# Optimization experiments

Measured on AMD Instinct MI355X. Metric: run time of the kernel, lower is better.

## Reference

```python
import jax, jax.numpy as jnp
import numpy as np

H, W, C = 1080, 1920, 3


def setup_inputs() -> dict:
    key = jax.random.key(0)
    k1, k2, k3 = jax.random.split(key, 3)
    img = jax.random.normal(k1, (H, W, C), dtype=jnp.float32)
    # ~10px typical displacement for realistic optical flow
    flow = jax.random.normal(k2, (1, H, W, 2), dtype=jnp.float32) * 10.0
    # depths in [0.1, 80); no pixel hits the 100.0 invalid sentinel
    depth = jax.random.uniform(k3, (H, W), dtype=jnp.float32, minval=0.1, maxval=80.0)
    return {"img": img, "flow": flow, "depth": depth, "split": 10}


def reference(img, flow, depth, split):
    # Depth-ordered forward-warping splat (z-buffer style compositing).
    # kernel_size=1 -> nearest-neighbor splat: each source pixel (y,x) writes
    # its value to (round(y+flow_y), round(x+flow_x)); passes go far->near and
    # nearer (nonzero) writes overwrite farther ones.
    flow = flow[0]                      # [H, W, 2], (dx, dy)
    h, w, c = img.shape

    # midpoints of the depth histogram, excluding the 100.0 invalid sentinel
    valid = depth != 100.0
    sd = jnp.sort(jnp.where(valid, depth, jnp.inf).ravel())
    l = valid.sum()
    step = l // split
    mids = jnp.concatenate(
        [jnp.take(sd, jnp.arange(split) * step), jnp.take(sd, l - 1)[None]]
    )  # [split+1], ascending

    ys, xs = jnp.meshgrid(jnp.arange(h), jnp.arange(w), indexing="ij")
    ty = jnp.round(ys + flow[..., 1]).astype(jnp.int32)   # target row
    tx = jnp.round(xs + flow[..., 0]).astype(jnp.int32)   # target col

    res = jnp.zeros_like(img)
    for i in range(split, 0, -1):       # far bin first, near bin last
        dmask = (depth < mids[i]) & (depth >= mids[i - 1])   # [H, W]
        # pixels outside the bin scatter to row h -> dropped (mode='drop')
        ty_i = jnp.where(dmask, ty, h)
        out = jnp.zeros_like(img).at[ty_i, tx].set(
            img * dmask[..., None].astype(img.dtype), mode="drop"
        )
        # nearer nonzero splats overwrite; zeros keep previous content
        res = res * (out == 0) + out
    return res
```

## Files before the change

kernel.cpp:

```cpp
#include <hip/hip_runtime.h>

typedef unsigned int u32;

static constexpr int HH = 1080, WW = 1920;
static constexpr int NPIX = HH * WW;
static constexpr int NQ = 17;
static constexpr int MAXOWN = 16;
static constexpr int OPB = 4;
static constexpr int NGRP = MAXOWN / OPB;
static constexpr int NBLK = 512;
static constexpr int BT   = 1024;
static constexpr int R1 = 16;
static constexpr int NCH1 = 64;
static constexpr int TS = 64;
static constexpr int TCX = WW / TS;
static constexpr int TCY = (HH + TS - 1) / TS;
static constexpr int NTILE = TCX * TCY;
static constexpr int NT512 = 512;

static constexpr size_t MIDS_OFF  = 0;
static constexpr size_t QB1_OFF   = 128;
static constexpr size_t QR1_OFF   = 256;
static constexpr size_t OIDX_OFF  = 384;
static constexpr size_t OBIN_OFF  = 512;
static constexpr size_t NOWN_OFF  = 640;
static constexpr size_t KEY22_OFF = 768;
static constexpr size_t R2O_OFF   = 896;
static constexpr size_t TOT1_OFF  = 1024;
static constexpr size_t GH2_OFF   = TOT1_OFF + (size_t)R1 * 4096 * 4;
static constexpr size_t ZERO_BYTES = GH2_OFF + (size_t)NQ * 1024 * 4;
static constexpr size_t TCNT_OFF  = ZERO_BYTES;
static constexpr size_t TTOT_OFF  = TCNT_OFF + (size_t)NBLK * NT512 * 4;
static constexpr size_t TBASE_OFF = TTOT_OFF + NT512 * 4;
static constexpr size_t TEND_OFF  = TBASE_OFF + NT512 * 4;
static constexpr size_t BASE2_OFF = TEND_OFF + NT512 * 4;
static constexpr size_t GH1_OFF   = BASE2_OFF + (size_t)NBLK * NT512 * 4;
static constexpr size_t PAIRS_OFF = GH1_OFF + (size_t)MAXOWN * NCH1 * 1024 * 4;

static constexpr int ZVEC = (int)(ZERO_BYTES / 16);
static constexpr int ZBLK = (ZVEC + 255) / 256;

__global__ __launch_bounds__(256) void k_zero(float4* __restrict__ ws) {
    int i = blockIdx.x * 256 + threadIdx.x;
    if (i < ZVEC) ws[i] = make_float4(0.f, 0.f, 0.f, 0.f);
}

__device__ __forceinline__ int target_of(int y, int x, float fx, float fy) {
    int ty = (int)rintf((float)y + fy);
    int tx = (int)rintf((float)x + fx);
    if (ty < 0) ty += HH;
    if (tx < 0) tx += WW;
    if ((unsigned)ty >= (unsigned)HH || (unsigned)tx >= (unsigned)WW) return -1;
    return ty * WW + tx;
}

__global__ __launch_bounds__(BT) void k_histA_cnt(const float* __restrict__ depth,
                                                  const float* __restrict__ flow,
                                                  u32* __restrict__ tot1,
                                                  u32* __restrict__ tcnt) {
    __shared__ u32 h[4096];
    __shared__ u32 tc[NT512];
    int tid = threadIdx.x;
    for (int j = tid; j < 4096; j += BT) h[j] = 0;
    for (int j = tid; j < NT512; j += BT) tc[j] = 0;
    __syncthreads();
    const int nvec = NPIX / 4;
    for (int v = blockIdx.x * BT + tid; v < nvec; v += gridDim.x * BT) {
        int i = v * 4;
        float4 d4 = ((const float4*)depth)[v];
        float4 fa = ((const float4*)flow)[v * 2];
        float4 fb = ((const float4*)flow)[v * 2 + 1];
        int y = i / WW, x0 = i - y * WW;
        float dd[4] = {d4.x, d4.y, d4.z, d4.w};
        float fx[4] = {fa.x, fa.z, fb.x, fb.z};
        float fy[4] = {fa.y, fa.w, fb.y, fb.w};
        #pragma unroll
        for (int j = 0; j < 4; ++j) {
            if (dd[j] != 100.0f)
                atomicAdd(&h[__float_as_uint(dd[j]) >> 20], 1u);
            int t = target_of(y, x0 + j, fx[j], fy[j]);
            if (t >= 0) {
                int ty = t / WW, tx = t - ty * WW;
                atomicAdd(&tc[(ty >> 6) * TCX + (tx >> 6)], 1u);
            }
        }
    }
    __syncthreads();
    u32 rep = blockIdx.x & (R1 - 1);
    for (int j = tid; j < 4096; j += BT) {
        u32 v = h[j];
        if (v) atomicAdd(&tot1[rep * 4096 + j], v);
    }
    for (int j = tid; j < NT512; j += BT)
        tcnt[blockIdx.x * NT512 + j] = tc[j];
}

__global__ __launch_bounds__(NBLK) void k_tscan(const u32* __restrict__ tcnt,
                                                u32* __restrict__ ttot,
                                                u32* __restrict__ base2) {
    __shared__ u32 s[NBLK];
    int t = blockIdx.x, b = threadIdx.x;
    u32 v = tcnt[b * NT512 + t];
    s[b] = v;
    __syncthreads();
    for (int off = 1; off < NBLK; off <<= 1) {
        u32 x = (b >= off) ? s[b - off] : 0;
        __syncthreads();
        s[b] += x;
        __syncthreads();
    }
    base2[b * NT512 + t] = s[b] - v;
    if (b == NBLK - 1) ttot[t] = s[NBLK - 1];
}

__global__ __launch_bounds__(1024) void k_selA(const u32* __restrict__ tot1,
                                               const int* __restrict__ splitp,
                                               const u32* __restrict__ ttot,
                                               u32* __restrict__ qb1, u32* __restrict__ qr1,
                                               u32* __restrict__ oidx, u32* __restrict__ obin,
                                               u32* __restrict__ nown,
                                               u32* __restrict__ tbase, u32* __restrict__ tend) {
    __shared__ u32 part[1024];
    __shared__ u32 qbS[NQ], qcS[NQ];
    __shared__ u32 totalsh;
    int tid = threadIdx.x;
    int split = *splitp;
    int base = tid * 4;
    u32 cc[4] = {0, 0, 0, 0};
    for (int r = 0; r < R1; ++r)
        for (int j = 0; j < 4; ++j) cc[j] += tot1[r * 4096 + base + j];
    u32 local = cc[0] + cc[1] + cc[2] + cc[3];
    part[tid] = local;
    __syncthreads();
    for (int off = 1; off < 1024; off <<= 1) {
        u32 v = (tid >= off) ? part[tid - off] : 0;
        __syncthreads();
        part[tid] += v;
        __syncthreads();
    }
    if (tid == 1023) totalsh = part[1023];
    __syncthreads();
    u32 l = totalsh;
    u32 step = l / (u32)split;
    u32 cum = part[tid] - local;
    for (int j = 0; j < 4; ++j) {
        u32 c = cc[j];
        if (c) {
            for (int q = 0; q <= split; ++q) {
                u32 r = (q < split) ? (u32)q * step : l - 1u;
                if (r >= cum && r < cum + c) {
                    qb1[q] = (u32)(base + j);
                    qr1[q] = r - cum;
                    qbS[q] = (u32)(base + j);
                    qcS[q] = c;
                }
            }
        }
        cum += c;
    }
    __syncthreads();
    if (tid == 0) {
        int w = -1;
        u32 prev = 0xFFFFFFFFu;
        for (int q = 0; q <= split; ++q) {
            if (qbS[q] != prev) { ++w; prev = qbS[q]; obin[w] = qbS[q]; }
            oidx[q] = (u32)w;
        }
        for (int w2 = w + 1; w2 < MAXOWN; ++w2) obin[w2] = 0xFFFFFFFFu;
        *nown = (u32)(w + 1);
    }
    __syncthreads();
    u32 tv = (tid < NT512) ? ttot[tid] : 0;
    part[tid] = tv;
    __syncthreads();
    for (int off = 1; off < 1024; off <<= 1) {
        u32 v = (tid >= off) ? part[tid - off] : 0;
        __syncthreads();
        part[tid] += v;
        __syncthreads();
    }
    if (tid < NT512) {
        tbase[tid] = part[tid] - tv;
        tend[tid]  = part[tid];
    }
}

__global__ __launch_bounds__(1024) void k_ph1(const float* __restrict__ depth,
                                              const u32* __restrict__ obin,
                                              const u32* __restrict__ nownp,
                                              u32* __restrict__ ghist) {
    int c = blockIdx.x / NGRP;
    int g = blockIdx.x % NGRP;
    int w0 = g * OPB;
    int nown = (int)*nownp;
    if (w0 >= nown) return;
    __shared__ u32 h[OPB * 1024];
    int tid = threadIdx.x;
    u32 ob[OPB];
    #pragma unroll
    for (int k = 0; k < OPB; ++k)
        ob[k] = (w0 + k < nown) ? obin[w0 + k] : 0xFFFFFFFFu;
    for (int j = tid; j < OPB * 1024; j += 1024) h[j] = 0;
    __syncthreads();
    const int per = (NPIX / 4) / NCH1;
    int lo = c * per, hi = lo + per;
    for (int v = lo + tid; v < hi; v += 1024) {
        float4 d4 = ((const float4*)depth)[v];
        float dd[4] = {d4.x, d4.y, d4.z, d4.w};
        #pragma unroll
        for (int j = 0; j < 4; ++j) {
            u32 bits = __float_as_uint(dd[j]);
            u32 b1 = bits >> 20;
            #pragma unroll
            for (int k = 0; k < OPB; ++k)
                if (ob[k] == b1)
                    atomicAdd(&h[k * 1024 + ((bits >> 10) & 1023u)], 1u);
        }
    }
    __syncthreads();
    for (int j = tid; j < OPB * 1024; j += 1024) {
        int k = j >> 10, bin = j & 1023;
        int w = w0 + k;
        if (w < nown) ghist[(w * NCH1 + c) * 1024 + bin] = h[j];
    }
}

__global__ __launch_bounds__(1024) void k_red1(const int* __restrict__ splitp,
                                               const u32* __restrict__ qb1,
                                               const u32* __restrict__ qr1,
                                               const u32* __restrict__ oidx,
                                               const u32* __restrict__ ghist,
                                               u32* __restrict__ key22, u32* __restrict__ r2o) {
    int q = blockIdx.x;
    if (q > *splitp) return;
    int w = (int)oidx[q];
    __shared__ u32 part[1024];
    int tid = threadIdx.x;
    u32 local = 0;
    for (int c = 0; c < NCH1; ++c) local += ghist[(w * NCH1 + c) * 1024 + tid];
    part[tid] = local;
    __syncthreads();
    for (int off = 1; off < 1024; off <<= 1) {
        u32 v = (tid >= off) ? part[tid - off] : 0;
        __syncthreads();
        part[tid] += v;
        __syncthreads();
    }
    u32 target = qr1[q];
    u32 cum = part[tid] - local;
    if (local && target >= cum && target < cum + local) {
        key22[q] = (qb1[q] << 10) | (u32)tid;
        r2o[q] = target - cum;
    }
}

__global__ __launch_bounds__(256) void k_ph2(const float* __restrict__ depth,
                                             const int* __restrict__ splitp,
                                             const u32* __restrict__ key22,
                                             u32* __restrict__ gh2) {
    __shared__ u32 k22[NQ];
    int tid = threadIdx.x, split = *splitp;
    if (tid < NQ) k22[tid] = (tid <= split) ? key22[tid] : 0xFFFFFFFFu;
    __syncthreads();
    const int nvec = NPIX / 4;
    for (int v = blockIdx.x * blockDim.x + tid; v < nvec; v += gridDim.x * blockDim.x) {
        float4 d4 = ((const float4*)depth)[v];
        float dd[4] = {d4.x, d4.y, d4.z, d4.w};
        #pragma unroll
        for (int j = 0; j < 4; ++j) {
            if (dd[j] != 100.0f) {
                u32 bits = __float_as_uint(dd[j]);
                u32 hi22 = bits >> 10;
                for (int q = 0; q <= split; ++q)
                    if (k22[q] == hi22) atomicAdd(&gh2[q * 1024 + (bits & 1023u)], 1u);
            }
        }
    }
}

__global__ __launch_bounds__(1024) void k_red2(const int* __restrict__ splitp,
                                               const u32* __restrict__ key22,
                                               const u32* __restrict__ r2o,
                                               const u32* __restrict__ gh2,
                                               float* __restrict__ mids) {
    int q = blockIdx.x;
    if (q > *splitp) return;
    __shared__ u32 part[1024];
    int tid = threadIdx.x;
    u32 local = gh2[q * 1024 + tid];
    part[tid] = local;
    __syncthreads();
    for (int off = 1; off < 1024; off <<= 1) {
        u32 v = (tid >= off) ? part[tid - off] : 0;
        __syncthreads();
        part[tid] += v;
        __syncthreads();
    }
    u32 target = r2o[q];
    u32 cum = part[tid] - local;
    if (local && target >= cum && target < cum + local)
        mids[q] = __uint_as_float((key22[q] << 10) | (u32)tid);
}

__global__ __launch_bounds__(BT) void k_scatter(const float* __restrict__ depth,
                                                const float* __restrict__ flow,
                                                const int* __restrict__ splitp,
                                                const float* __restrict__ mids,
                                                const u32* __restrict__ tbase,
                                                const u32* __restrict__ base2,
                                                uint2* __restrict__ pairs) {
    __shared__ u32 cur[NT512];
    __shared__ float msh[NQ];
    int tid = threadIdx.x, split = *splitp;
    if (tid < NQ) msh[tid] = (tid <= split) ? mids[tid] : 0.f;
    for (int j = tid; j < NT512; j += BT)
        cur[j] = tbase[j] + base2[blockIdx.x * NT512 + j];
    __syncthreads();
    const int nvec = NPIX / 4;
    for (int v = blockIdx.x * BT + tid; v < nvec; v += gridDim.x * BT) {
        int i = v * 4;
        float4 d4 = ((const float4*)depth)[v];
        float4 fa = ((const float4*)flow)[v * 2];
        float4 fb = ((const float4*)flow)[v * 2 + 1];
        int y = i / WW, x0 = i - y * WW;
        float dd[4] = {d4.x, d4.y, d4.z, d4.w};
        float fx[4] = {fa.x, fa.z, fb.x, fb.z};
        float fy[4] = {fa.y, fa.w, fb.y, fb.w};
        #pragma unroll
        for (int j = 0; j < 4; ++j) {
            int t = target_of(y, x0 + j, fx[j], fy[j]);
            if (t < 0) continue;
            float d = dd[j];
            int rank = -1;
            for (int k = 1; k <= split; ++k)
                if (d >= msh[k - 1] && d < msh[k]) { rank = split - k; break; }
            u32 p = (rank >= 0) ? (u32)rank * (u32)NPIX + (u32)(i + j) + 1u : 0u;
            int ty = t / WW, tx = t - ty * WW;
            int tile = (ty >> 6) * TCX + (tx >> 6);
            u32 pos = atomicAdd(&cur[tile], 1u);
            pairs[pos] = make_uint2((u32)t, p);
        }
    }
}

__global__ __launch_bounds__(1024) void k_tile_reduce(const uint2* __restrict__ pairs,
                                                      const u32* __restrict__ tbase,
                                                      const u32* __restrict__ tend,
                                                      const float* __restrict__ img,
                                                      float* __restrict__ out) {
    __shared__ u32 zb[TS * TS];
    int tid = threadIdx.x;
    int tile = blockIdx.x;
    for (int c = tid; c < TS * TS; c += 1024) zb[c] = 0;
    __syncthreads();
    int ty0 = (tile / TCX) << 6, tx0 = (tile % TCX) << 6;
    u32 b = tbase[tile], e = tend[tile];
    for (u32 k = b + tid; k < e; k += 1024) {
        uint2 pr = pairs[k];
        int t = (int)pr.x;
        int ty = t / WW, tx = t - ty * WW;
        atomicMax(&zb[((ty - ty0) << 6) | (tx - tx0)], pr.y);
    }
    __syncthreads();
    for (int c = tid; c < TS * TS; c += 1024) {
        int ty = ty0 + (c >> 6);
        if (ty >= HH) continue;
        int tx = tx0 + (c & 63);
        u32 p = zb[c];
        float r = 0.f, g = 0.f, bl = 0.f;
        if (p) {
            u32 src = (p - 1u) % (u32)NPIX;
            r  = img[src * 3 + 0];
            g  = img[src * 3 + 1];
            bl = img[src * 3 + 2];
        }
        int t = ty * WW + tx;
        out[t * 3 + 0] = r;
        out[t * 3 + 1] = g;
        out[t * 3 + 2] = bl;
    }
}

extern "C" void kernel_launch(void* const* d_in, const int* in_sizes, int n_in,
                              void* d_out, int out_size, void* d_ws, size_t ws_size,
                              hipStream_t stream) {
    const float* img    = (const float*)d_in[0];
    const float* flow   = (const float*)d_in[1];
    const float* depth  = (const float*)d_in[2];
    const int*   splitp = (const int*)d_in[3];

    char* ws = (char*)d_ws;
    float* mids  = (float*)(ws + MIDS_OFF);
    u32*   qb1   = (u32*)(ws + QB1_OFF);
    u32*   qr1   = (u32*)(ws + QR1_OFF);
    u32*   oidx  = (u32*)(ws + OIDX_OFF);
    u32*   obin  = (u32*)(ws + OBIN_OFF);
    u32*   nown  = (u32*)(ws + NOWN_OFF);
    u32*   key22 = (u32*)(ws + KEY22_OFF);
    u32*   r2o   = (u32*)(ws + R2O_OFF);
    u32*   tot1  = (u32*)(ws + TOT1_OFF);
    u32*   gh2   = (u32*)(ws + GH2_OFF);
    u32*   tcnt  = (u32*)(ws + TCNT_OFF);
    u32*   ttot  = (u32*)(ws + TTOT_OFF);
    u32*   tbase = (u32*)(ws + TBASE_OFF);
    u32*   tend  = (u32*)(ws + TEND_OFF);
    u32*   base2 = (u32*)(ws + BASE2_OFF);
    u32*   gh1   = (u32*)(ws + GH1_OFF);
    uint2* pairs = (uint2*)(ws + PAIRS_OFF);
    float* out   = (float*)d_out;

    k_zero       <<<ZBLK, 256, 0, stream>>>((float4*)d_ws);
    k_histA_cnt  <<<NBLK, BT, 0, stream>>>(depth, flow, tot1, tcnt);
    k_tscan      <<<NT512, NBLK, 0, stream>>>(tcnt, ttot, base2);
    k_selA       <<<1, 1024, 0, stream>>>(tot1, splitp, ttot, qb1, qr1, oidx, obin, nown, tbase, tend);
    k_ph1        <<<NCH1 * NGRP, 1024, 0, stream>>>(depth, obin, nown, gh1);
    k_red1       <<<NQ, 1024, 0, stream>>>(splitp, qb1, qr1, oidx, gh1, key22, r2o);
    k_ph2        <<<2048, 256, 0, stream>>>(depth, splitp, key22, gh2);
    k_red2       <<<NQ, 1024, 0, stream>>>(splitp, key22, r2o, gh2, mids);
    k_scatter    <<<NBLK, BT, 0, stream>>>(depth, flow, splitp, mids, tbase, base2, pairs);
    k_tile_reduce<<<NTILE, 1024, 0, stream>>>(pairs, tbase, tend, img, out);
}
```

Measured before the change: 95.81 us.

## Fuse tile counting, scan and scatter into per-block staged segments

Drops the separate tile-count pass and global tile scan. Each block now counts its pixels per tile, scans those counts in shared memory, stages its (target, priority) pairs in LDS and writes them to its own fixed segment. The tile reducer then gathers from every block's segment using per-block counts and offsets. This removes one full pass over depth and flow, the scan kernel and the scattered global writes. The price is a serial per-thread loop over segments in the reducer, with only a few threads active per tile, and the ph1 chunking knobs are retuned.

New measurement: 104.2 us. 8.7% more time.

```diff
diff --git a/kernel.cpp b/kernel.cpp
--- a/kernel.cpp
+++ b/kernel.cpp
@@ -4,14 +4,16 @@
 
 static constexpr int HH = 1080, WW = 1920;
 static constexpr int NPIX = HH * WW;
+static constexpr int NVEC = NPIX / 4;
 static constexpr int NQ = 17;
 static constexpr int MAXOWN = 16;
-static constexpr int OPB = 4;
+static constexpr int OPB = 8;
 static constexpr int NGRP = MAXOWN / OPB;
 static constexpr int NBLK = 512;
 static constexpr int BT   = 1024;
+static constexpr int SEG  = 4096;
 static constexpr int R1 = 16;
-static constexpr int NCH1 = 64;
+static constexpr int NCH1 = 128;
 static constexpr int TS = 64;
 static constexpr int TCX = WW / TS;
 static constexpr int TCY = (HH + TS - 1) / TS;
@@ -30,10 +32,7 @@
 static constexpr size_t GH2_OFF   = TOT1_OFF + (size_t)R1 * 4096 * 4;
 static constexpr size_t ZERO_BYTES = GH2_OFF + (size_t)NQ * 1024 * 4;
 static constexpr size_t TCNT_OFF  = ZERO_BYTES;
-static constexpr size_t TTOT_OFF  = TCNT_OFF + (size_t)NBLK * NT512 * 4;
-static constexpr size_t TBASE_OFF = TTOT_OFF + NT512 * 4;
-static constexpr size_t TEND_OFF  = TBASE_OFF + NT512 * 4;
-static constexpr size_t BASE2_OFF = TEND_OFF + NT512 * 4;
+static constexpr size_t BASE2_OFF = TCNT_OFF + (size_t)NBLK * NT512 * 4;
 static constexpr size_t GH1_OFF   = BASE2_OFF + (size_t)NBLK * NT512 * 4;
 static constexpr size_t PAIRS_OFF = GH1_OFF + (size_t)MAXOWN * NCH1 * 1024 * 4;
 
@@ -54,36 +53,19 @@
     return ty * WW + tx;
 }
 
-__global__ __launch_bounds__(BT) void k_histA_cnt(const float* __restrict__ depth,
-                                                  const float* __restrict__ flow,
-                                                  u32* __restrict__ tot1,
-                                                  u32* __restrict__ tcnt) {
+__global__ __launch_bounds__(BT) void k_histQ(const float* __restrict__ depth,
+                                              u32* __restrict__ tot1) {
     __shared__ u32 h[4096];
-    __shared__ u32 tc[NT512];
     int tid = threadIdx.x;
     for (int j = tid; j < 4096; j += BT) h[j] = 0;
-    for (int j = tid; j < NT512; j += BT) tc[j] = 0;
-    __syncthreads();
-    const int nvec = NPIX / 4;
-    for (int v = blockIdx.x * BT + tid; v < nvec; v += gridDim.x * BT) {
-        int i = v * 4;
+    __syncthreads();
+    for (int v = blockIdx.x * BT + tid; v < NVEC; v += gridDim.x * BT) {
         float4 d4 = ((const float4*)depth)[v];
-        float4 fa = ((const float4*)flow)[v * 2];
-        float4 fb = ((const float4*)flow)[v * 2 + 1];
-        int y = i / WW, x0 = i - y * WW;
         float dd[4] = {d4.x, d4.y, d4.z, d4.w};
-        float fx[4] = {fa.x, fa.z, fb.x, fb.z};
-        float fy[4] = {fa.y, fa.w, fb.y, fb.w};
         #pragma unroll
-        for (int j = 0; j < 4; ++j) {
+        for (int j = 0; j < 4; ++j)
             if (dd[j] != 100.0f)
                 atomicAdd(&h[__float_as_uint(dd[j]) >> 20], 1u);
-            int t = target_of(y, x0 + j, fx[j], fy[j]);
-            if (t >= 0) {
-                int ty = t / WW, tx = t - ty * WW;
-                atomicAdd(&tc[(ty >> 6) * TCX + (tx >> 6)], 1u);
-            }
-        }
     }
     __syncthreads();
     u32 rep = blockIdx.x & (R1 - 1);
@@ -91,37 +73,15 @@
         u32 v = h[j];
         if (v) atomicAdd(&tot1[rep * 4096 + j], v);
     }
-    for (int j = tid; j < NT512; j += BT)
-        tcnt[blockIdx.x * NT512 + j] = tc[j];
-}
-
-__global__ __launch_bounds__(NBLK) void k_tscan(const u32* __restrict__ tcnt,
-                                                u32* __restrict__ ttot,
-                                                u32* __restrict__ base2) {
-    __shared__ u32 s[NBLK];
-    int t = blockIdx.x, b = threadIdx.x;
-    u32 v = tcnt[b * NT512 + t];
-    s[b] = v;
-    __syncthreads();
-    for (int off = 1; off < NBLK; off <<= 1) {
-        u32 x = (b >= off) ? s[b - off] : 0;
-        __syncthreads();
-        s[b] += x;
-        __syncthreads();
-    }
-    base2[b * NT512 + t] = s[b] - v;
-    if (b == NBLK - 1) ttot[t] = s[NBLK - 1];
 }
 
 __global__ __launch_bounds__(1024) void k_selA(const u32* __restrict__ tot1,
                                                const int* __restrict__ splitp,
-                                               const u32* __restrict__ ttot,
                                                u32* __restrict__ qb1, u32* __restrict__ qr1,
                                                u32* __restrict__ oidx, u32* __restrict__ obin,
-                                               u32* __restrict__ nown,
-                                               u32* __restrict__ tbase, u32* __restrict__ tend) {
+                                               u32* __restrict__ nown) {
     __shared__ u32 part[1024];
-    __shared__ u32 qbS[NQ], qcS[NQ];
+    __shared__ u32 qbS[NQ];
     __shared__ u32 totalsh;
     int tid = threadIdx.x;
     int split = *splitp;
@@ -152,7 +112,6 @@
                     qb1[q] = (u32)(base + j);
                     qr1[q] = r - cum;
                     qbS[q] = (u32)(base + j);
-                    qcS[q] = c;
                 }
             }
         }
@@ -168,20 +127,6 @@
         }
         for (int w2 = w + 1; w2 < MAXOWN; ++w2) obin[w2] = 0xFFFFFFFFu;
         *nown = (u32)(w + 1);
-    }
-    __syncthreads();
-    u32 tv = (tid < NT512) ? ttot[tid] : 0;
-    part[tid] = tv;
-    __syncthreads();
-    for (int off = 1; off < 1024; off <<= 1) {
-        u32 v = (tid >= off) ? part[tid - off] : 0;
-        __syncthreads();
-        part[tid] += v;
-        __syncthreads();
-    }
-    if (tid < NT512) {
-        tbase[tid] = part[tid] - tv;
-        tend[tid]  = part[tid];
     }
 }
 
@@ -202,7 +147,7 @@
         ob[k] = (w0 + k < nown) ? obin[w0 + k] : 0xFFFFFFFFu;
     for (int j = tid; j < OPB * 1024; j += 1024) h[j] = 0;
     __syncthreads();
-    const int per = (NPIX / 4) / NCH1;
+    const int per = NVEC / NCH1;
     int lo = c * per, hi = lo + per;
     for (int v = lo + tid; v < hi; v += 1024) {
         float4 d4 = ((const float4*)depth)[v];
@@ -262,8 +207,7 @@
     int tid = threadIdx.x, split = *splitp;
     if (tid < NQ) k22[tid] = (tid <= split) ? key22[tid] : 0xFFFFFFFFu;
     __syncthreads();
-    const int nvec = NPIX / 4;
-    for (int v = blockIdx.x * blockDim.x + tid; v < nvec; v += gridDim.x * blockDim.x) {
+    for (int v = blockIdx.x * blockDim.x + tid; v < NVEC; v += gridDim.x * blockDim.x) {
         float4 d4 = ((const float4*)depth)[v];
         float dd[4] = {d4.x, d4.y, d4.z, d4.w};
         #pragma unroll
@@ -302,22 +246,30 @@
         mids[q] = __uint_as_float((key22[q] << 10) | (u32)tid);
 }
 
-__global__ __launch_bounds__(BT) void k_scatter(const float* __restrict__ depth,
-                                                const float* __restrict__ flow,
-                                                const int* __restrict__ splitp,
-                                                const float* __restrict__ mids,
-                                                const u32* __restrict__ tbase,
-                                                const u32* __restrict__ base2,
-                                                uint2* __restrict__ pairs) {
+__global__ __launch_bounds__(BT) void k_build(const float* __restrict__ depth,
+                                              const float* __restrict__ flow,
+                                              const int* __restrict__ splitp,
+                                              const float* __restrict__ mids,
+                                              u32* __restrict__ tcnt,
+                                              u32* __restrict__ base2,
+                                              uint2* __restrict__ pairs) {
+    __shared__ u32 tc[NT512];
+    __shared__ u32 s[NT512];
     __shared__ u32 cur[NT512];
+    __shared__ uint2 stage[SEG];
     __shared__ float msh[NQ];
-    int tid = threadIdx.x, split = *splitp;
+    __shared__ u32 total_sh;
+    int tid = threadIdx.x;
+    int split = *splitp;
     if (tid < NQ) msh[tid] = (tid <= split) ? mids[tid] : 0.f;
-    for (int j = tid; j < NT512; j += BT)
-        cur[j] = tbase[j] + base2[blockIdx.x * NT512 + j];
-    __syncthreads();
-    const int nvec = NPIX / 4;
-    for (int v = blockIdx.x * BT + tid; v < nvec; v += gridDim.x * BT) {
+    if (tid < NT512) tc[tid] = 0;
+    __syncthreads();
+    int v = blockIdx.x * BT + tid;
+    int tt[4];
+    u32 pp[4] = {0, 0, 0, 0};
+    #pragma unroll
+    for (int j = 0; j < 4; ++j) tt[j] = -1;
+    if (v < NVEC) {
         int i = v * 4;
         float4 d4 = ((const float4*)depth)[v];
         float4 fa = ((const float4*)flow)[v * 2];
@@ -329,37 +281,76 @@
         #pragma unroll
         for (int j = 0; j < 4; ++j) {
             int t = target_of(y, x0 + j, fx[j], fy[j]);
-            if (t < 0) continue;
-            float d = dd[j];
-            int rank = -1;
-            for (int k = 1; k <= split; ++k)
-                if (d >= msh[k - 1] && d < msh[k]) { rank = split - k; break; }
-            u32 p = (rank >= 0) ? (u32)rank * (u32)NPIX + (u32)(i + j) + 1u : 0u;
+            tt[j] = t;
+            if (t >= 0) {
+                float d = dd[j];
+                int rank = -1;
+                for (int k = 1; k <= split; ++k)
+                    if (d >= msh[k - 1] && d < msh[k]) { rank = split - k; break; }
+                pp[j] = (rank >= 0) ? (u32)rank * (u32)NPIX + (u32)(i + j) + 1u : 0u;
+                int ty = t / WW, tx = t - ty * WW;
+                atomicAdd(&tc[(ty >> 6) * TCX + (tx >> 6)], 1u);
+            }
+        }
+    }
+    __syncthreads();
+    if (tid < NT512) s[tid] = tc[tid];
+    __syncthreads();
+    for (int off = 1; off < NT512; off <<= 1) {
+        u32 x = (tid < NT512 && tid >= off) ? s[tid - off] : 0;
+        __syncthreads();
+        if (tid < NT512) s[tid] += x;
+        __syncthreads();
+    }
+    if (tid < NT512) {
+        u32 c = tc[tid];
+        u32 b = s[tid] - c;
+        tcnt[blockIdx.x * NT512 + tid]  = c;
+        base2[blockIdx.x * NT512 + tid] = b;
+        cur[tid] = b;
+    }
+    if (tid == NT512 - 1) total_sh = s[NT512 - 1];
+    __syncthreads();
+    #pragma unroll
+    for (int j = 0; j < 4; ++j) {
+        if (tt[j] >= 0) {
+            int t = tt[j];
             int ty = t / WW, tx = t - ty * WW;
-            int tile = (ty >> 6) * TCX + (tx >> 6);
-            u32 pos = atomicAdd(&cur[tile], 1u);
-            pairs[pos] = make_uint2((u32)t, p);
-        }
-    }
+            u32 pos = atomicAdd(&cur[(ty >> 6) * TCX + (tx >> 6)], 1u);
+            stage[pos] = make_uint2((u32)t, pp[j]);
+        }
+    }
+    __syncthreads();
+    u32 total = total_sh;
+    uint2* segp = pairs + (size_t)blockIdx.x * SEG;
+    for (u32 j = tid; j < total; j += BT) segp[j] = stage[j];
 }
 
 __global__ __launch_bounds__(1024) void k_tile_reduce(const uint2* __restrict__ pairs,
-                                                      const u32* __restrict__ tbase,
-                                                      const u32* __restrict__ tend,
+                                                      const u32* __restrict__ tcnt,
+                                                      const u32* __restrict__ base2,
                                                       const float* __restrict__ img,
                                                       float* __restrict__ out) {
     __shared__ u32 zb[TS * TS];
+    __shared__ u32 cnt_l[NT512], off_l[NT512];
     int tid = threadIdx.x;
     int tile = blockIdx.x;
     for (int c = tid; c < TS * TS; c += 1024) zb[c] = 0;
+    if (tid < NT512) {
+        cnt_l[tid] = tcnt[tid * NT512 + tile];
+        off_l[tid] = base2[tid * NT512 + tile];
+    }
     __syncthreads();
     int ty0 = (tile / TCX) << 6, tx0 = (tile % TCX) << 6;
-    u32 b = tbase[tile], e = tend[tile];
-    for (u32 k = b + tid; k < e; k += 1024) {
-        uint2 pr = pairs[k];
-        int t = (int)pr.x;
-        int ty = t / WW, tx = t - ty * WW;
-        atomicMax(&zb[((ty - ty0) << 6) | (tx - tx0)], pr.y);
+    if (tid < NT512) {
+        u32 c = cnt_l[tid];
+        const uint2* segp = pairs + (size_t)tid * SEG + off_l[tid];
+        for (u32 k = 0; k < c; ++k) {
+            uint2 pr = segp[k];
+            int t = (int)pr.x;
+            int ty = t / WW, tx = t - ty * WW;
+            atomicMax(&zb[((ty - ty0) << 6) | (tx - tx0)], pr.y);
+        }
     }
     __syncthreads();
     for (int c = tid; c < TS * TS; c += 1024) {
@@ -401,22 +392,18 @@
     u32*   tot1  = (u32*)(ws + TOT1_OFF);
     u32*   gh2   = (u32*)(ws + GH2_OFF);
     u32*   tcnt  = (u32*)(ws + TCNT_OFF);
-    u32*   ttot  = (u32*)(ws + TTOT_OFF);
-    u32*   tbase = (u32*)(ws + TBASE_OFF);
-    u32*   tend  = (u32*)(ws + TEND_OFF);
     u32*   base2 = (u32*)(ws + BASE2_OFF);
     u32*   gh1   = (u32*)(ws + GH1_OFF);
     uint2* pairs = (uint2*)(ws + PAIRS_OFF);
     float* out   = (float*)d_out;
 
     k_zero       <<<ZBLK, 256, 0, stream>>>((float4*)d_ws);
-    k_histA_cnt  <<<NBLK, BT, 0, stream>>>(depth, flow, tot1, tcnt);
-    k_tscan      <<<NT512, NBLK, 0, stream>>>(tcnt, ttot, base2);
-    k_selA       <<<1, 1024, 0, stream>>>(tot1, splitp, ttot, qb1, qr1, oidx, obin, nown, tbase, tend);
+    k_histQ      <<<NBLK, BT, 0, stream>>>(depth, tot1);
+    k_selA       <<<1, 1024, 0, stream>>>(tot1, splitp, qb1, qr1, oidx, obin, nown);
     k_ph1        <<<NCH1 * NGRP, 1024, 0, stream>>>(depth, obin, nown, gh1);
     k_red1       <<<NQ, 1024, 0, stream>>>(splitp, qb1, qr1, oidx, gh1, key22, r2o);
     k_ph2        <<<2048, 256, 0, stream>>>(depth, splitp, key22, gh2);
     k_red2       <<<NQ, 1024, 0, stream>>>(splitp, key22, r2o, gh2, mids);
-    k_scatter    <<<NBLK, BT, 0, stream>>>(depth, flow, splitp, mids, tbase, base2, pairs);
-    k_tile_reduce<<<NTILE, 1024, 0, stream>>>(pairs, tbase, tend, img, out);
-}
+    k_build      <<<NBLK, BT, 0, stream>>>(depth, flow, splitp, mids, tcnt, base2, pairs);
+    k_tile_reduce<<<NTILE, 1024, 0, stream>>>(pairs, tcnt, base2, img, out);
+}
```

## Merge tile scan with bin selection and move tile-base scan into red1

Applied to the files above, without the earlier changes.

Merges the per-tile prefix-scan kernel and the single-block selection kernel into one launch, where the extra block does the bin selection with 512 threads handling 8 bins each. The global tile-base scan moves into an extra block of the k_red1 launch, so one kernel launch and one serial dependency step are removed. It also retunes phase-1 histogram parameters (8 owners per block, 128 chunks). The gh1 buffer layout changes with NCH1 and must still fit the workspace, and k_red1 now sums twice as many chunks per bin.

Measured after the change: 95.17 us, median of 2. Within noise of the previous version (-0.7%).

```diff
diff --git a/kernel.cpp b/kernel.cpp
--- a/kernel.cpp
+++ b/kernel.cpp
@@ -4,14 +4,16 @@
 
 static constexpr int HH = 1080, WW = 1920;
 static constexpr int NPIX = HH * WW;
+static constexpr int NVEC = NPIX / 4;
 static constexpr int NQ = 17;
 static constexpr int MAXOWN = 16;
-static constexpr int OPB = 4;
+static constexpr int OPB = 8;
 static constexpr int NGRP = MAXOWN / OPB;
 static constexpr int NBLK = 512;
 static constexpr int BT   = 1024;
 static constexpr int R1 = 16;
-static constexpr int NCH1 = 64;
+static constexpr int NCH1 = 128;
+static constexpr int CH1V = NVEC / NCH1;
 static constexpr int TS = 64;
 static constexpr int TCX = WW / TS;
 static constexpr int TCY = (HH + TS - 1) / TS;
@@ -64,8 +66,7 @@
     for (int j = tid; j < 4096; j += BT) h[j] = 0;
     for (int j = tid; j < NT512; j += BT) tc[j] = 0;
     __syncthreads();
-    const int nvec = NPIX / 4;
-    for (int v = blockIdx.x * BT + tid; v < nvec; v += gridDim.x * BT) {
+    for (int v = blockIdx.x * BT + tid; v < NVEC; v += gridDim.x * BT) {
         int i = v * 4;
         float4 d4 = ((const float4*)depth)[v];
         float4 fa = ((const float4*)flow)[v * 2];
@@ -95,64 +96,67 @@
         tcnt[blockIdx.x * NT512 + j] = tc[j];
 }
 
-__global__ __launch_bounds__(NBLK) void k_tscan(const u32* __restrict__ tcnt,
-                                                u32* __restrict__ ttot,
-                                                u32* __restrict__ base2) {
-    __shared__ u32 s[NBLK];
-    int t = blockIdx.x, b = threadIdx.x;
-    u32 v = tcnt[b * NT512 + t];
-    s[b] = v;
-    __syncthreads();
-    for (int off = 1; off < NBLK; off <<= 1) {
-        u32 x = (b >= off) ? s[b - off] : 0;
-        __syncthreads();
-        s[b] += x;
-        __syncthreads();
-    }
-    base2[b * NT512 + t] = s[b] - v;
-    if (b == NBLK - 1) ttot[t] = s[NBLK - 1];
-}
-
-__global__ __launch_bounds__(1024) void k_selA(const u32* __restrict__ tot1,
-                                               const int* __restrict__ splitp,
-                                               const u32* __restrict__ ttot,
-                                               u32* __restrict__ qb1, u32* __restrict__ qr1,
-                                               u32* __restrict__ oidx, u32* __restrict__ obin,
-                                               u32* __restrict__ nown,
-                                               u32* __restrict__ tbase, u32* __restrict__ tend) {
-    __shared__ u32 part[1024];
-    __shared__ u32 qbS[NQ], qcS[NQ];
+__global__ __launch_bounds__(512) void k_scan_sel(const u32* __restrict__ tcnt,
+                                                  const u32* __restrict__ tot1,
+                                                  const int* __restrict__ splitp,
+                                                  u32* __restrict__ ttot, u32* __restrict__ base2,
+                                                  u32* __restrict__ qb1, u32* __restrict__ qr1,
+                                                  u32* __restrict__ oidx, u32* __restrict__ obin,
+                                                  u32* __restrict__ nown) {
+    __shared__ u32 s[512];
+    __shared__ u32 qbS[NQ];
     __shared__ u32 totalsh;
     int tid = threadIdx.x;
+    if (blockIdx.x < NT512) {
+        int t = blockIdx.x;
+        u32 v = tcnt[tid * NT512 + t];
+        s[tid] = v;
+        __syncthreads();
+        for (int off = 1; off < 512; off <<= 1) {
+            u32 x = (tid >= off) ? s[tid - off] : 0;
+            __syncthreads();
+            s[tid] += x;
+            __syncthreads();
+        }
+        base2[tid * NT512 + t] = s[tid] - v;
+        if (tid == 511) ttot[t] = s[511];
+        return;
+    }
     int split = *splitp;
-    int base = tid * 4;
-    u32 cc[4] = {0, 0, 0, 0};
-    for (int r = 0; r < R1; ++r)
-        for (int j = 0; j < 4; ++j) cc[j] += tot1[r * 4096 + base + j];
-    u32 local = cc[0] + cc[1] + cc[2] + cc[3];
-    part[tid] = local;
-    __syncthreads();
-    for (int off = 1; off < 1024; off <<= 1) {
-        u32 v = (tid >= off) ? part[tid - off] : 0;
-        __syncthreads();
-        part[tid] += v;
-        __syncthreads();
-    }
-    if (tid == 1023) totalsh = part[1023];
+    int base = tid * 8;
+    u32 cc[8];
+    #pragma unroll
+    for (int k = 0; k < 8; ++k) cc[k] = 0;
+    for (int r = 0; r < R1; ++r) {
+        const u32* tp = tot1 + r * 4096 + base;
+        #pragma unroll
+        for (int k = 0; k < 8; ++k) cc[k] += tp[k];
+    }
+    u32 local = 0;
+    #pragma unroll
+    for (int k = 0; k < 8; ++k) local += cc[k];
+    s[tid] = local;
+    __syncthreads();
+    for (int off = 1; off < 512; off <<= 1) {
+        u32 x = (tid >= off) ? s[tid - off] : 0;
+        __syncthreads();
+        s[tid] += x;
+        __syncthreads();
+    }
+    if (tid == 511) totalsh = s[511];
     __syncthreads();
     u32 l = totalsh;
     u32 step = l / (u32)split;
-    u32 cum = part[tid] - local;
-    for (int j = 0; j < 4; ++j) {
-        u32 c = cc[j];
+    u32 cum = s[tid] - local;
+    for (int k = 0; k < 8; ++k) {
+        u32 c = cc[k];
         if (c) {
             for (int q = 0; q <= split; ++q) {
                 u32 r = (q < split) ? (u32)q * step : l - 1u;
                 if (r >= cum && r < cum + c) {
-                    qb1[q] = (u32)(base + j);
+                    qb1[q] = (u32)(base + k);
                     qr1[q] = r - cum;
-                    qbS[q] = (u32)(base + j);
-                    qcS[q] = c;
+                    qbS[q] = (u32)(base + k);
                 }
             }
         }
@@ -168,20 +172,6 @@
         }
         for (int w2 = w + 1; w2 < MAXOWN; ++w2) obin[w2] = 0xFFFFFFFFu;
         *nown = (u32)(w + 1);
-    }
-    __syncthreads();
-    u32 tv = (tid < NT512) ? ttot[tid] : 0;
-    part[tid] = tv;
-    __syncthreads();
-    for (int off = 1; off < 1024; off <<= 1) {
-        u32 v = (tid >= off) ? part[tid - off] : 0;
-        __syncthreads();
-        part[tid] += v;
-        __syncthreads();
-    }
-    if (tid < NT512) {
-        tbase[tid] = part[tid] - tv;
-        tend[tid]  = part[tid];
     }
 }
 
@@ -202,8 +192,7 @@
         ob[k] = (w0 + k < nown) ? obin[w0 + k] : 0xFFFFFFFFu;
     for (int j = tid; j < OPB * 1024; j += 1024) h[j] = 0;
     __syncthreads();
-    const int per = (NPIX / 4) / NCH1;
-    int lo = c * per, hi = lo + per;
+    int lo = c * CH1V, hi = lo + CH1V;
     for (int v = lo + tid; v < hi; v += 1024) {
         float4 d4 = ((const float4*)depth)[v];
         float dd[4] = {d4.x, d4.y, d4.z, d4.w};
@@ -230,27 +219,45 @@
                                                const u32* __restrict__ qr1,
                                                const u32* __restrict__ oidx,
                                                const u32* __restrict__ ghist,
-                                               u32* __restrict__ key22, u32* __restrict__ r2o) {
-    int q = blockIdx.x;
-    if (q > *splitp) return;
-    int w = (int)oidx[q];
+                                               const u32* __restrict__ ttot,
+                                               u32* __restrict__ key22, u32* __restrict__ r2o,
+                                               u32* __restrict__ tbase, u32* __restrict__ tend) {
     __shared__ u32 part[1024];
     int tid = threadIdx.x;
+    int b = blockIdx.x;
+    if (b == NQ) {
+        u32 tv = (tid < NT512) ? ttot[tid] : 0;
+        part[tid] = tv;
+        __syncthreads();
+        for (int off = 1; off < 1024; off <<= 1) {
+            u32 x = (tid >= off) ? part[tid - off] : 0;
+            __syncthreads();
+            part[tid] += x;
+            __syncthreads();
+        }
+        if (tid < NT512) {
+            tbase[tid] = part[tid] - tv;
+            tend[tid]  = part[tid];
+        }
+        return;
+    }
+    if (b > *splitp) return;
+    int w = (int)oidx[b];
     u32 local = 0;
     for (int c = 0; c < NCH1; ++c) local += ghist[(w * NCH1 + c) * 1024 + tid];
     part[tid] = local;
     __syncthreads();
     for (int off = 1; off < 1024; off <<= 1) {
-        u32 v = (tid >= off) ? part[tid - off] : 0;
-        __syncthreads();
-        part[tid] += v;
-        __syncthreads();
-    }
-    u32 target = qr1[q];
+        u32 x = (tid >= off) ? part[tid - off] : 0;
+        __syncthreads();
+        part[tid] += x;
+        __syncthreads();
+    }
+    u32 target = qr1[b];
     u32 cum = part[tid] - local;
     if (local && target >= cum && target < cum + local) {
-        key22[q] = (qb1[q] << 10) | (u32)tid;
-        r2o[q] = target - cum;
+        key22[b] = (qb1[b] << 10) | (u32)tid;
+        r2o[b] = target - cum;
     }
 }
 
@@ -262,8 +269,7 @@
     int tid = threadIdx.x, split = *splitp;
     if (tid < NQ) k22[tid] = (tid <= split) ? key22[tid] : 0xFFFFFFFFu;
     __syncthreads();
-    const int nvec = NPIX / 4;
-    for (int v = blockIdx.x * blockDim.x + tid; v < nvec; v += gridDim.x * blockDim.x) {
+    for (int v = blockIdx.x * blockDim.x + tid; v < NVEC; v += gridDim.x * blockDim.x) {
         float4 d4 = ((const float4*)depth)[v];
         float dd[4] = {d4.x, d4.y, d4.z, d4.w};
         #pragma unroll
@@ -313,11 +319,9 @@
     __shared__ float msh[NQ];
     int tid = threadIdx.x, split = *splitp;
     if (tid < NQ) msh[tid] = (tid <= split) ? mids[tid] : 0.f;
-    for (int j = tid; j < NT512; j += BT)
-        cur[j] = tbase[j] + base2[blockIdx.x * NT512 + j];
-    __syncthreads();
-    const int nvec = NPIX / 4;
-    for (int v = blockIdx.x * BT + tid; v < nvec; v += gridDim.x * BT) {
+    if (tid < NT512) cur[tid] = tbase[tid] + base2[blockIdx.x * NT512 + tid];
+    __syncthreads();
+    for (int v = blockIdx.x * BT + tid; v < NVEC; v += gridDim.x * BT) {
         int i = v * 4;
         float4 d4 = ((const float4*)depth)[v];
         float4 fa = ((const float4*)flow)[v * 2];
@@ -411,10 +415,11 @@
 
     k_zero       <<<ZBLK, 256, 0, stream>>>((float4*)d_ws);
     k_histA_cnt  <<<NBLK, BT, 0, stream>>>(depth, flow, tot1, tcnt);
-    k_tscan      <<<NT512, NBLK, 0, stream>>>(tcnt, ttot, base2);
-    k_selA       <<<1, 1024, 0, stream>>>(tot1, splitp, ttot, qb1, qr1, oidx, obin, nown, tbase, tend);
+    k_scan_sel   <<<NT512 + 1, 512, 0, stream>>>(tcnt, tot1, splitp, ttot, base2,
+                                                 qb1, qr1, oidx, obin, nown);
     k_ph1        <<<NCH1 * NGRP, 1024, 0, stream>>>(depth, obin, nown, gh1);
-    k_red1       <<<NQ, 1024, 0, stream>>>(splitp, qb1, qr1, oidx, gh1, key22, r2o);
+    k_red1       <<<NQ + 1, 1024, 0, stream>>>(splitp, qb1, qr1, oidx, gh1, ttot,
+                                               key22, r2o, tbase, tend);
     k_ph2        <<<2048, 256, 0, stream>>>(depth, splitp, key22, gh2);
     k_red2       <<<NQ, 1024, 0, stream>>>(splitp, key22, r2o, gh2, mids);
     k_scatter    <<<NBLK, BT, 0, stream>>>(depth, flow, splitp, mids, tbase, base2, pairs);
```
